# Kernel tuning notes

Hardware: AMD Instinct MI355X
Metric: run time of the kernel (lower is better)

The kernel has to match this reference:

```python
import jax, jax.numpy as jnp
import numpy as np

N, D, H, B, E = 100000, 256, 256, 128, 128
STEPS = 5


def setup_inputs() -> dict:
    key = jax.random.key(0)
    ks = jax.random.split(key, 16)
    w = lambda i, shape: (jax.random.normal(ks[i], shape, jnp.float32) * 0.05)
    inp = {
        "x": jax.random.normal(ks[0], (N, D), jnp.float32),
        "batch_idxs": jnp.sort(jax.random.randint(ks[1], (N,), 0, B)),
        # FNN: Linear(D,H) -> ELU -> Linear(H,H)
        "fnn_W1": w(2, (D, H)), "fnn_b1": jnp.zeros((H,), jnp.float32),
        "fnn_W2": w(3, (H, H)), "fnn_b2": jnp.zeros((H,), jnp.float32),
        # 3-layer LSTM, input 2H (layer 0) / H (layers 1,2), hidden H
        "Wih0": w(4, (4 * H, 2 * H)), "Whh0": w(5, (4 * H, H)),
        "bih0": jnp.zeros((4 * H,), jnp.float32), "bhh0": jnp.zeros((4 * H,), jnp.float32),
        "Wih1": w(6, (4 * H, H)), "Whh1": w(7, (4 * H, H)),
        "bih1": jnp.zeros((4 * H,), jnp.float32), "bhh1": jnp.zeros((4 * H,), jnp.float32),
        "Wih2": w(8, (4 * H, H)), "Whh2": w(9, (4 * H, H)),
        "bih2": jnp.zeros((4 * H,), jnp.float32), "bhh2": jnp.zeros((4 * H,), jnp.float32),
        # output Linear(2H, E)
        "out_W": w(10, (2 * H, E)), "out_b": jnp.zeros((E,), jnp.float32),
    }
    return inp


def _lstm_cell(xin, h, c, Wih, Whh, bih, bhh):
    gates = xin @ Wih.T + bih + h @ Whh.T + bhh  # (B, 4H)
    i, f, g, o = jnp.split(gates, 4, axis=-1)    # PyTorch gate order i,f,g,o
    c = jax.nn.sigmoid(f) * c + jax.nn.sigmoid(i) * jnp.tanh(g)
    h = jax.nn.sigmoid(o) * jnp.tanh(c)
    return h, c


def reference(x, batch_idxs, fnn_W1, fnn_b1, fnn_W2, fnn_b2,
              Wih0, Whh0, bih0, bhh0, Wih1, Whh1, bih1, bhh1,
              Wih2, Whh2, bih2, bhh2, out_W, out_b):
    # FNN (ELU between layers)
    hfeat = jax.nn.elu(x @ fnn_W1 + fnn_b1) @ fnn_W2 + fnn_b2  # (N, H)

    Wihs, Whhs = (Wih0, Wih1, Wih2), (Whh0, Whh1, Whh2)
    bihs, bhhs = (bih0, bih1, bih2), (bhh0, bhh1, bhh2)
    hs = [jnp.zeros((B, H), hfeat.dtype) for _ in range(3)]
    cs = [jnp.zeros((B, H), hfeat.dtype) for _ in range(3)]
    q_star = jnp.zeros((B, 2 * H), hfeat.dtype)

    for _ in range(STEPS):
        layer_in = q_star
        for l in range(3):
            hs[l], cs[l] = _lstm_cell(layer_in, hs[l], cs[l], Wihs[l], Whhs[l], bihs[l], bhhs[l])
            layer_in = hs[l]
        q = layer_in  # (B, H)
        # segment (per-graph) attention softmax over nodes
        e = jnp.sum(hfeat * q[batch_idxs], axis=-1)                     # (N,)
        m = jax.ops.segment_max(e, batch_idxs, num_segments=B)
        m = jnp.where(jnp.isfinite(m), m, 0.0)                          # guard empty segments
        ex = jnp.exp(e - m[batch_idxs])
        denom = jax.ops.segment_sum(ex, batch_idxs, num_segments=B) + 1e-16
        a = ex / denom[batch_idxs]                                      # (N,)
        r = jax.ops.segment_sum(a[:, None] * hfeat, batch_idxs, num_segments=B)  # (B, H)
        q_star = jnp.concatenate([q, r], axis=-1)                       # (B, 2H)

    return q_star @ out_W + out_b  # (B, E)
```

## Files before the change

kernel.cpp:

```cpp
#include <hip/hip_runtime.h>

#define NN 100000
#define NSTEP 5
#define LSTR 264

typedef unsigned short ushort_t;
typedef __attribute__((ext_vector_type(8))) short short8;
typedef __attribute__((ext_vector_type(4))) float floatx4;

__device__ __forceinline__ ushort_t f2bf(float f){
  union { float f; unsigned u; } v; v.f = f;
  unsigned r = v.u + 0x7fffu + ((v.u >> 16) & 1u);
  return (ushort_t)(r >> 16);
}
__device__ __forceinline__ float bf2f(ushort_t s){
  union { unsigned u; float f; } v; v.u = ((unsigned)s) << 16;
  return v.f;
}
__device__ __forceinline__ float sigf(float x){ return 1.0f/(1.0f+__expf(-x)); }

__global__ __launch_bounds__(512) void fnn_fused(const float* __restrict__ x,
    const ushort_t* __restrict__ W1P, const float* __restrict__ b1,
    const ushort_t* __restrict__ W2P, const float* __restrict__ b2,
    ushort_t* __restrict__ hfeat, int M)
{
  __shared__ ushort_t buf[64 * LSTR];
  int tid = threadIdx.x;
  int w = tid >> 6, lane = tid & 63, qd = lane >> 4, r16 = lane & 15;
  int row0 = blockIdx.x * 64;
  int col0 = w * 32;

  floatx4 acc[4][2];
  short8 afA[4], afB[4], bfA[2], bfB[2];

  auto LDA = [&](short8* d, int kc){
    #pragma unroll
    for (int i=0;i<4;i++) d[i] = *(const short8*)&buf[(i*16 + r16)*LSTR + kc*32 + qd*8];
  };
  auto LDW = [&](short8* d, const ushort_t* P, int kc){
    #pragma unroll
    for (int j=0;j<2;j++) d[j] = *(const short8*)(P + (size_t)(((w*2 + j)*8 + kc)*64 + lane)*8);
  };
  auto MM = [&](short8* a, short8* b){
    #pragma unroll
    for (int i=0;i<4;i++)
      #pragma unroll
      for (int j=0;j<2;j++)
        acc[i][j] = __builtin_amdgcn_mfma_f32_16x16x32_bf16(a[i], b[j], acc[i][j], 0, 0, 0);
  };

  {
    float4 xv[8];
    #pragma unroll
    for (int it = 0; it < 8; it++){
      int idx = it * 512 + tid;
      int rg = row0 + (idx >> 6); if (rg >= M) rg = M - 1;
      xv[it] = *(const float4*)(x + (size_t)rg * 256 + (idx & 63) * 4);
    }
    #pragma unroll
    for (int it = 0; it < 8; it++){
      int idx = it * 512 + tid;
      ushort4 pk = make_ushort4(f2bf(xv[it].x), f2bf(xv[it].y), f2bf(xv[it].z), f2bf(xv[it].w));
      *(ushort4*)&buf[(idx >> 6) * LSTR + (idx & 63) * 4] = pk;
    }
  }
  LDW(bfA, W1P, 0);
  __syncthreads();

  #pragma unroll
  for (int i=0;i<4;i++)
    #pragma unroll
    for (int j=0;j<2;j++) acc[i][j] = (floatx4){0.f,0.f,0.f,0.f};
  LDA(afA, 0);
  #pragma unroll
  for (int kc = 0; kc < 8; kc += 2){
    if (kc + 1 < 8){ LDA(afB, kc+1); LDW(bfB, W1P, kc+1); }
    MM(afA, bfA);
    if (kc + 2 < 8){ LDA(afA, kc+2); LDW(bfA, W1P, kc+2); }
    if (kc + 1 < 8) MM(afB, bfB);
  }
  __syncthreads();

  LDW(bfA, W2P, 0);
  #pragma unroll
  for (int i=0;i<4;i++){
    #pragma unroll
    for (int j=0;j<2;j++){
      int col = col0 + j*16 + r16;
      float bb = b1[col];
      #pragma unroll
      for (int rr=0;rr<4;rr++){
        int row = i*16 + qd*4 + rr;
        float v = acc[i][j][rr] + bb;
        v = v > 0.f ? v : (__expf(v) - 1.0f);
        buf[row * LSTR + col] = f2bf(v);
      }
    }
  }
  __syncthreads();

  #pragma unroll
  for (int i=0;i<4;i++)
    #pragma unroll
    for (int j=0;j<2;j++) acc[i][j] = (floatx4){0.f,0.f,0.f,0.f};
  LDA(afA, 0);
  #pragma unroll
  for (int kc = 0; kc < 8; kc += 2){
    if (kc + 1 < 8){ LDA(afB, kc+1); LDW(bfB, W2P, kc+1); }
    MM(afA, bfA);
    if (kc + 2 < 8){ LDA(afA, kc+2); LDW(bfA, W2P, kc+2); }
    if (kc + 1 < 8) MM(afB, bfB);
  }

  #pragma unroll
  for (int i=0;i<4;i++){
    #pragma unroll
    for (int j=0;j<2;j++){
      int col = col0 + j*16 + r16;
      float bb = b2[col];
      #pragma unroll
      for (int rr=0;rr<4;rr++){
        int row = row0 + i*16 + qd*4 + rr;
        if (row < M) hfeat[(size_t)row * 256 + col] = f2bf(acc[i][j][rr] + bb);
      }
    }
  }
}

template<int KC, bool FIN>
__global__ __launch_bounds__(256, 1) void lstm_layer(const ushort_t* __restrict__ A,
    const ushort_t* __restrict__ WcP, const float* __restrict__ bcp,
    float* __restrict__ c, ushort_t* __restrict__ dstA, int sA,
    ushort_t* __restrict__ dstB, int sB, float* __restrict__ qdst,
    const float* __restrict__ r_part, const float* __restrict__ z_part)
{
  __shared__ float sbuf[3][4][256];
  __shared__ ushort_t shr[16][264];
  constexpr int lda = KC * 32;
  constexpr int kcq = KC >> 2;
  int tid = threadIdx.x, w = tid >> 6, lane = tid & 63, qd = lane >> 4, r16 = lane & 15;
  int m0 = (blockIdx.x & 7) * 16, nt = blockIdx.x >> 3;

  if (FIN){
    int col = tid;
    #pragma unroll 4
    for (int r = 0; r < 16; r++){
      int bb = m0 + r;
      const float* rp = r_part + ((size_t)bb*256 + col)*8;
      float4 aa = *(const float4*)rp;
      float4 ab = *(const float4*)(rp + 4);
      float s = aa.x+aa.y+aa.z+aa.w + ab.x+ab.y+ab.z+ab.w;
      const float* zp = z_part + bb*8;
      float4 za = *(const float4*)zp;
      float4 zb = *(const float4*)(zp + 4);
      float z = za.x+za.y+za.z+za.w + zb.x+zb.y+zb.z+zb.w;
      shr[r][col] = f2bf(s / (z + 1e-16f));
    }
    __syncthreads();
  }

  int kc0 = w * kcq;
  floatx4 acc[4];
  #pragma unroll
  for (int g=0; g<4; g++) acc[g] = (floatx4){0.f,0.f,0.f,0.f};

  const ushort_t* Ar = A + (size_t)(m0 + r16) * lda + qd * 8;
  #pragma unroll
  for (int kk = 0; kk < kcq; kk++){
    int kc = kc0 + kk;
    short8 av;
    if (FIN && kc >= 8 && kc < 16)
      av = *(const short8*)&shr[r16][(kc - 8)*32 + qd*8];
    else
      av = *(const short8*)(Ar + kc*32);
    #pragma unroll
    for (int g = 0; g < 4; g++){
      short8 bv = *(const short8*)(WcP + (size_t)((((g*16 + nt)*KC) + kc)*64 + lane)*8);
      acc[g] = __builtin_amdgcn_mfma_f32_16x16x32_bf16(av, bv, acc[g], 0, 0, 0);
    }
  }
  if (w){
    #pragma unroll
    for (int g=0; g<4; g++) *(floatx4*)&sbuf[w-1][g][lane*4] = acc[g];
  }
  __syncthreads();
  if (w == 0){
    #pragma unroll
    for (int g=0; g<4; g++)
      #pragma unroll
      for (int t=0; t<3; t++){
        floatx4 p = *(floatx4*)&sbuf[t][g][lane*4];
        acc[g] = acc[g] + p;
      }
    int h = nt*16 + r16;
    float bci = bcp[h], bcf = bcp[256+h], bcg = bcp[512+h], bco = bcp[768+h];
    #pragma unroll
    for (int rr=0; rr<4; rr++){
      int row = m0 + qd*4 + rr;
      float gi = acc[0][rr] + bci;
      float gf = acc[1][rr] + bcf;
      float gg = acc[2][rr] + bcg;
      float go = acc[3][rr] + bco;
      float cp = c[row*256 + h];
      float cn = sigf(gf)*cp + sigf(gi)*tanhf(gg);
      float hn = sigf(go)*tanhf(cn);
      c[row*256 + h] = cn;
      ushort_t hb = f2bf(hn);
      dstA[row*sA + h] = hb;
      dstB[row*sB + h] = hb;
      if (qdst) qdst[row*512 + h] = hn;
    }
  }
}

__global__ __launch_bounds__(256) void attn_onepass(const ushort_t* __restrict__ hfeat,
    const int* __restrict__ seg, const float* __restrict__ q_star,
    float* __restrict__ r_part, float* __restrict__ z_part)
{
  __shared__ float sred[4][260];
  int b = blockIdx.x >> 3, p = blockIdx.x & 7;
  int w = threadIdx.x >> 6, lane = threadIdx.x & 63;
  int s0 = seg[b], s1 = seg[b+1], len = s1 - s0;
  int q0 = s0 + ((len * p) >> 3);
  int q1 = s0 + ((len * (p+1)) >> 3);

  float S0=0.f, S1=0.f, S2=0.f, S3=0.f, Z=0.f;
  float4 q = *(const float4*)(q_star + (size_t)b*512 + lane*4);

  ushort4 cur[4];
  int base = q0 + w;
  #pragma unroll
  for (int u=0;u<4;u++){
    int n = base + 4*u;
    cur[u] = (n < q1) ? *(const ushort4*)(hfeat + (size_t)n*256 + lane*4)
                      : make_ushort4(0,0,0,0);
  }
  for (; base < q1; base += 16){
    ushort4 nxt[4];
    #pragma unroll
    for (int u=0;u<4;u++){
      int n = base + 16 + 4*u;
      nxt[u] = (n < q1) ? *(const ushort4*)(hfeat + (size_t)n*256 + lane*4) : cur[u];
    }
    float fv[4][4], d[4];
    #pragma unroll
    for (int u=0;u<4;u++){
      fv[u][0]=bf2f(cur[u].x); fv[u][1]=bf2f(cur[u].y);
      fv[u][2]=bf2f(cur[u].z); fv[u][3]=bf2f(cur[u].w);
      d[u] = fv[u][0]*q.x + fv[u][1]*q.y + fv[u][2]*q.z + fv[u][3]*q.w;
    }
    #pragma unroll
    for (int off = 32; off; off >>= 1){
      #pragma unroll
      for (int u=0;u<4;u++) d[u] += __shfl_xor(d[u], off);
    }
    #pragma unroll
    for (int u=0;u<4;u++){
      if (base + 4*u < q1){
        float wt = __expf(d[u]);
        Z += wt;
        S0 += wt*fv[u][0]; S1 += wt*fv[u][1];
        S2 += wt*fv[u][2]; S3 += wt*fv[u][3];
      }
    }
    #pragma unroll
    for (int u=0;u<4;u++) cur[u] = nxt[u];
  }

  *(float4*)&sred[w][lane*4] = (float4){S0, S1, S2, S3};
  if (lane == 0) sred[w][256] = Z;
  __syncthreads();
  int f = threadIdx.x;
  if (f < 256){
    float v = sred[0][f] + sred[1][f] + sred[2][f] + sred[3][f];
    r_part[((size_t)b*256 + f)*8 + p] = v;
    if (f == 0)
      z_part[b*8 + p] = sred[0][256] + sred[1][256] + sred[2][256] + sred[3][256];
  }
}

__global__ __launch_bounds__(256) void attn_fin(const float* __restrict__ r_part,
    const float* __restrict__ z_part, const float* __restrict__ q_star,
    const float* __restrict__ outW, const float* __restrict__ outb,
    float* __restrict__ out)
{
  __shared__ float qs[512];
  int b = blockIdx.x, f = threadIdx.x;
  const float* rp = r_part + ((size_t)b*256 + f)*8;
  float4 aa = *(const float4*)rp;
  float4 ab = *(const float4*)(rp + 4);
  float s = aa.x+aa.y+aa.z+aa.w + ab.x+ab.y+ab.z+ab.w;
  const float* zp = z_part + b*8;
  float4 za = *(const float4*)zp;
  float4 zb = *(const float4*)(zp + 4);
  float z = za.x+za.y+za.z+za.w + zb.x+zb.y+zb.z+zb.w;
  qs[256 + f] = s / (z + 1e-16f);
  qs[f] = q_star[b*512 + f];
  __syncthreads();
  if (f < 128){
    float acc = outb[f];
    for (int k = 0; k < 512; k++) acc += qs[k] * outW[k*128 + f];
    out[b*128 + f] = acc;
  }
}

__global__ void prep_all(const float* __restrict__ W1, const float* __restrict__ W2,
    const float* __restrict__ Wih0, const float* __restrict__ Whh0,
    const float* __restrict__ Wih1, const float* __restrict__ Whh1,
    const float* __restrict__ Wih2, const float* __restrict__ Whh2,
    const float* __restrict__ bih0, const float* __restrict__ bhh0,
    const float* __restrict__ bih1, const float* __restrict__ bhh1,
    const float* __restrict__ bih2, const float* __restrict__ bhh2,
    const int* __restrict__ bidx,
    ushort_t* __restrict__ W1P, ushort_t* __restrict__ W2P,
    ushort_t* __restrict__ Wc0P, ushort_t* __restrict__ Wc1P, ushort_t* __restrict__ Wc2P,
    float* __restrict__ c, ushort_t* __restrict__ xc, float* __restrict__ q_star,
    float* __restrict__ bc, int* __restrict__ seg)
{
  int i = blockIdx.x*256 + threadIdx.x;
  if (i < 131072){
    const float* W = (i < 65536) ? W1 : W2;
    ushort_t* P = (i < 65536) ? W1P : W2P;
    int r = i & 65535;
    int T = r >> 12, r2 = r & 4095;
    int kc = r2 >> 9, l = (r2 >> 3) & 63, j = r2 & 7;
    int k = kc*32 + ((l>>4)<<3) + j;
    int n = T*16 + (l & 15);
    P[r] = f2bf(W[k*256 + n]);
    return;
  }
  i -= 131072;
  if (i < 786432){
    int T = i / 12288, r2 = i - T*12288;
    int kc = r2 >> 9, l = (r2 >> 3) & 63, j = r2 & 7;
    int k = kc*32 + ((l>>4)<<3) + j;
    int g = T >> 4, n = (T & 15)*16 + (l & 15);
    int row = g*256 + n;
    Wc0P[i] = f2bf(k < 512 ? Wih0[row*512 + k] : Whh0[row*256 + (k - 512)]);
    return;
  }
  i -= 786432;
  if (i < 1048576){
    const float* Wih = (i < 524288) ? Wih1 : Wih2;
    const float* Whh = (i < 524288) ? Whh1 : Whh2;
    ushort_t* P = (i < 524288) ? Wc1P : Wc2P;
    int r = i & 524287;
    int T = r >> 13, r2 = r & 8191;
    int kc = r2 >> 9, l = (r2 >> 3) & 63, j = r2 & 7;
    int k = kc*32 + ((l>>4)<<3) + j;
    int g = T >> 4, n = (T & 15)*16 + (l & 15);
    int row = g*256 + n;
    P[r] = f2bf(k < 256 ? Wih[row*256 + k] : Whh[row*256 + (k - 256)]);
    return;
  }
  i -= 1048576;
  if (i < 98304) { c[i] = 0.f; return; }
  i -= 98304;
  if (i < 229376) { xc[i] = 0; return; }
  i -= 229376;
  if (i < 65536) { q_star[i] = 0.f; return; }
  i -= 65536;
  if (i < 3072) {
    int l = i >> 10, g = i & 1023;
    const float* bi = (l == 0) ? bih0 : ((l == 1) ? bih1 : bih2);
    const float* bh = (l == 0) ? bhh0 : ((l == 1) ? bhh1 : bhh2);
    bc[i] = bi[g] + bh[g];
    return;
  }
  i -= 3072;
  if (i < 129) {
    int lo = 0, hi = NN;
    while (lo < hi){ int mid = (lo + hi) >> 1; if (bidx[mid] < i) lo = mid + 1; else hi = mid; }
    seg[i] = lo;
    return;
  }
}

extern "C" void kernel_launch(void* const* d_in, const int* in_sizes, int n_in,
                              void* d_out, int out_size, void* d_ws, size_t ws_size,
                              hipStream_t stream)
{
  const float* x    = (const float*)d_in[0];
  const int*   bidx = (const int*)  d_in[1];
  const float* W1   = (const float*)d_in[2];
  const float* b1   = (const float*)d_in[3];
  const float* W2   = (const float*)d_in[4];
  const float* b2   = (const float*)d_in[5];
  const float* Wih0 = (const float*)d_in[6];
  const float* Whh0 = (const float*)d_in[7];
  const float* bih0 = (const float*)d_in[8];
  const float* bhh0 = (const float*)d_in[9];
  const float* Wih1 = (const float*)d_in[10];
  const float* Whh1 = (const float*)d_in[11];
  const float* bih1 = (const float*)d_in[12];
  const float* bhh1 = (const float*)d_in[13];
  const float* Wih2 = (const float*)d_in[14];
  const float* Whh2 = (const float*)d_in[15];
  const float* bih2 = (const float*)d_in[16];
  const float* bhh2 = (const float*)d_in[17];
  const float* outW = (const float*)d_in[18];
  const float* outb = (const float*)d_in[19];

  char* p = (char*)d_ws;
  auto alloc = [&](size_t bytes)->char*{ char* r = p; p += (bytes + 255) & ~(size_t)255; return r; };
  ushort_t* hfeat  = (ushort_t*)alloc((size_t)NN*256*2);
  ushort_t* W1P    = (ushort_t*)alloc(65536*2);
  ushort_t* W2P    = (ushort_t*)alloc(65536*2);
  ushort_t* Wc0P   = (ushort_t*)alloc(786432*2);
  ushort_t* Wc1P   = (ushort_t*)alloc(524288*2);
  ushort_t* Wc2P   = (ushort_t*)alloc(524288*2);
  float*    bc     = (float*)   alloc(3072*4);
  float*    c_all  = (float*)   alloc(98304*4);
  ushort_t* xc     = (ushort_t*)alloc(229376*2);
  float*    q_star = (float*)   alloc(65536*4);
  float*    r_part = (float*)   alloc((size_t)128*256*8*4);
  float*    z_part = (float*)   alloc(128*8*4);
  int*      seg    = (int*)     alloc(129*4);

  ushort_t* xc0 = xc;
  ushort_t* xc1 = xc + 98304;
  ushort_t* xc2 = xc + 163840;
  float* c0 = c_all, *c1 = c_all + 32768, *c2 = c_all + 65536;
  float* bc0 = bc, *bc1 = bc + 1024, *bc2 = bc + 2048;

  prep_all<<<9229, 256, 0, stream>>>(W1, W2, Wih0, Whh0, Wih1, Whh1, Wih2, Whh2,
                                     bih0, bhh0, bih1, bhh1, bih2, bhh2, bidx,
                                     W1P, W2P, Wc0P, Wc1P, Wc2P,
                                     c_all, xc, q_star, bc, seg);

  fnn_fused<<<1563, 512, 0, stream>>>(x, W1P, b1, W2P, b2, hfeat, NN);

  for (int s = 0; s < NSTEP; s++){
    if (s == 0)
      lstm_layer<24,false><<<128, 256, 0, stream>>>(xc0, Wc0P, bc0, c0,
          xc0 + 512, 768, xc1, 512, nullptr, nullptr, nullptr);
    else
      lstm_layer<24,true><<<128, 256, 0, stream>>>(xc0, Wc0P, bc0, c0,
          xc0 + 512, 768, xc1, 512, nullptr, r_part, z_part);
    lstm_layer<16,false><<<128, 256, 0, stream>>>(xc1, Wc1P, bc1, c1,
        xc1 + 256, 512, xc2, 512, nullptr, nullptr, nullptr);
    lstm_layer<16,false><<<128, 256, 0, stream>>>(xc2, Wc2P, bc2, c2,
        xc2 + 256, 512, xc0, 768, q_star, nullptr, nullptr);
    attn_onepass<<<1024, 256, 0, stream>>>(hfeat, seg, q_star, r_part, z_part);
  }
  attn_fin<<<128, 256, 0, stream>>>(r_part, z_part, q_star, outW, outb, (float*)d_out);
}
```

Before: 448.1 us.

## Stage FNN weights into LDS via async global_load_lds with 32-row tiles

The fused FNN kernel now handles 32 rows per block instead of 64, doubling the grid to 3125 blocks. Weight fragments are streamed into a double-buffered LDS area with global_load_lds and manual vmcnt waits, instead of being loaded into registers. The second layer's weights are prefetched while the ELU epilogue runs. The tail bounds check is dropped because 100000 divides evenly by 32, and lstm_layer loses its min-blocks launch bound. The aim is more overlap of weight fetch with MFMA and higher occupancy, at the cost of less reuse of each weight fragment per block.

```diff
diff --git a/kernel.cpp b/kernel.cpp
--- a/kernel.cpp
+++ b/kernel.cpp
@@ -24,74 +24,94 @@
     const ushort_t* __restrict__ W2P, const float* __restrict__ b2,
     ushort_t* __restrict__ hfeat, int M)
 {
-  __shared__ ushort_t buf[64 * LSTR];
+  __shared__ ushort_t buf[32 * LSTR];
+  __shared__ ushort_t wst[2][8][2][512];
   int tid = threadIdx.x;
   int w = tid >> 6, lane = tid & 63, qd = lane >> 4, r16 = lane & 15;
-  int row0 = blockIdx.x * 64;
-  int col0 = w * 32;
-
-  floatx4 acc[4][2];
-  short8 afA[4], afB[4], bfA[2], bfB[2];
-
-  auto LDA = [&](short8* d, int kc){
-    #pragma unroll
-    for (int i=0;i<4;i++) d[i] = *(const short8*)&buf[(i*16 + r16)*LSTR + kc*32 + qd*8];
-  };
-  auto LDW = [&](short8* d, const ushort_t* P, int kc){
-    #pragma unroll
-    for (int j=0;j<2;j++) d[j] = *(const short8*)(P + (size_t)(((w*2 + j)*8 + kc)*64 + lane)*8);
-  };
-  auto MM = [&](short8* a, short8* b){
-    #pragma unroll
-    for (int i=0;i<4;i++)
-      #pragma unroll
-      for (int j=0;j<2;j++)
-        acc[i][j] = __builtin_amdgcn_mfma_f32_16x16x32_bf16(a[i], b[j], acc[i][j], 0, 0, 0);
-  };
+  size_t row0 = (size_t)blockIdx.x * 32;
+
+  typedef __attribute__((address_space(3))) unsigned int lds_u32;
+  typedef __attribute__((address_space(1))) const unsigned int glb_u32;
+
+  float bb1[2], bb2[2];
+  #pragma unroll
+  for (int j = 0; j < 2; j++){
+    int col = w*32 + j*16 + r16;
+    bb1[j] = b1[col];
+    bb2[j] = b2[col];
+  }
 
   {
-    float4 xv[8];
-    #pragma unroll
-    for (int it = 0; it < 8; it++){
+    float4 xv[4];
+    #pragma unroll
+    for (int it = 0; it < 4; it++){
       int idx = it * 512 + tid;
-      int rg = row0 + (idx >> 6); if (rg >= M) rg = M - 1;
-      xv[it] = *(const float4*)(x + (size_t)rg * 256 + (idx & 63) * 4);
-    }
-    #pragma unroll
-    for (int it = 0; it < 8; it++){
+      xv[it] = *(const float4*)(x + (row0 + (idx >> 6)) * 256 + (idx & 63) * 4);
+    }
+    #pragma unroll
+    for (int it = 0; it < 4; it++){
       int idx = it * 512 + tid;
       ushort4 pk = make_ushort4(f2bf(xv[it].x), f2bf(xv[it].y), f2bf(xv[it].z), f2bf(xv[it].w));
       *(ushort4*)&buf[(idx >> 6) * LSTR + (idx & 63) * 4] = pk;
     }
   }
-  LDW(bfA, W1P, 0);
-  __syncthreads();
-
-  #pragma unroll
-  for (int i=0;i<4;i++)
-    #pragma unroll
-    for (int j=0;j<2;j++) acc[i][j] = (floatx4){0.f,0.f,0.f,0.f};
-  LDA(afA, 0);
-  #pragma unroll
-  for (int kc = 0; kc < 8; kc += 2){
-    if (kc + 1 < 8){ LDA(afB, kc+1); LDW(bfB, W1P, kc+1); }
-    MM(afA, bfA);
-    if (kc + 2 < 8){ LDA(afA, kc+2); LDW(bfA, W1P, kc+2); }
-    if (kc + 1 < 8) MM(afB, bfB);
-  }
-  __syncthreads();
-
-  LDW(bfA, W2P, 0);
-  #pragma unroll
-  for (int i=0;i<4;i++){
+  __syncthreads();
+
+  auto STAGE = [&](const ushort_t* __restrict__ P, int kc, int ph){
+    #pragma unroll
+    for (int j = 0; j < 2; j++){
+      const ushort_t* gp = P + (size_t)(((w*2 + j)*8 + kc)*512) + lane*8;
+      __builtin_amdgcn_global_load_lds((glb_u32*)gp, (lds_u32*)&wst[ph][w][j][0], 16, 0, 0);
+    }
+  };
+
+  floatx4 acc[2][2];
+
+  auto GEMM = [&](const ushort_t* __restrict__ P, bool prestaged){
+    if (!prestaged){ STAGE(P, 0, 0); STAGE(P, 1, 1); }
+    #pragma unroll
+    for (int i=0;i<2;i++)
+      #pragma unroll
+      for (int j=0;j<2;j++) acc[i][j] = (floatx4){0.f,0.f,0.f,0.f};
+    #pragma unroll
+    for (int kc = 0; kc < 8; kc++){
+      int ph = kc & 1;
+      if (kc < 7) asm volatile("s_waitcnt vmcnt(2)" ::: "memory");
+      else        asm volatile("s_waitcnt vmcnt(0)" ::: "memory");
+      short8 af[2], bf[2];
+      #pragma unroll
+      for (int i=0;i<2;i++)
+        af[i] = *(const short8*)&buf[(i*16 + r16)*LSTR + kc*32 + qd*8];
+      #pragma unroll
+      for (int j=0;j<2;j++)
+        bf[j] = *(const short8*)&wst[ph][w][j][lane*8];
+      #pragma unroll
+      for (int i=0;i<2;i++)
+        #pragma unroll
+        for (int j=0;j<2;j++)
+          acc[i][j] = __builtin_amdgcn_mfma_f32_16x16x32_bf16(af[i], bf[j], acc[i][j], 0, 0, 0);
+      if (kc + 2 < 8){
+        asm volatile("s_waitcnt lgkmcnt(0)" ::: "memory");
+        STAGE(P, kc + 2, ph);
+      }
+    }
+  };
+
+  GEMM(W1P, false);
+
+  asm volatile("s_waitcnt lgkmcnt(0)" ::: "memory");
+  STAGE(W2P, 0, 0); STAGE(W2P, 1, 1);
+  __syncthreads();
+
+  #pragma unroll
+  for (int i=0;i<2;i++){
     #pragma unroll
     for (int j=0;j<2;j++){
-      int col = col0 + j*16 + r16;
-      float bb = b1[col];
+      int col = w*32 + j*16 + r16;
       #pragma unroll
       for (int rr=0;rr<4;rr++){
         int row = i*16 + qd*4 + rr;
-        float v = acc[i][j][rr] + bb;
+        float v = acc[i][j][rr] + bb1[j];
         v = v > 0.f ? v : (__expf(v) - 1.0f);
         buf[row * LSTR + col] = f2bf(v);
       }
@@ -99,36 +119,24 @@
   }
   __syncthreads();
 
-  #pragma unroll
-  for (int i=0;i<4;i++)
-    #pragma unroll
-    for (int j=0;j<2;j++) acc[i][j] = (floatx4){0.f,0.f,0.f,0.f};
-  LDA(afA, 0);
-  #pragma unroll
-  for (int kc = 0; kc < 8; kc += 2){
-    if (kc + 1 < 8){ LDA(afB, kc+1); LDW(bfB, W2P, kc+1); }
-    MM(afA, bfA);
-    if (kc + 2 < 8){ LDA(afA, kc+2); LDW(bfA, W2P, kc+2); }
-    if (kc + 1 < 8) MM(afB, bfB);
-  }
-
-  #pragma unroll
-  for (int i=0;i<4;i++){
+  GEMM(W2P, true);
+
+  #pragma unroll
+  for (int i=0;i<2;i++){
     #pragma unroll
     for (int j=0;j<2;j++){
-      int col = col0 + j*16 + r16;
-      float bb = b2[col];
+      int col = w*32 + j*16 + r16;
       #pragma unroll
       for (int rr=0;rr<4;rr++){
-        int row = row0 + i*16 + qd*4 + rr;
-        if (row < M) hfeat[(size_t)row * 256 + col] = f2bf(acc[i][j][rr] + bb);
+        size_t row = row0 + i*16 + qd*4 + rr;
+        hfeat[row * 256 + col] = f2bf(acc[i][j][rr] + bb2[j]);
       }
     }
   }
 }
 
 template<int KC, bool FIN>
-__global__ __launch_bounds__(256, 1) void lstm_layer(const ushort_t* __restrict__ A,
+__global__ __launch_bounds__(256) void lstm_layer(const ushort_t* __restrict__ A,
     const ushort_t* __restrict__ WcP, const float* __restrict__ bcp,
     float* __restrict__ c, ushort_t* __restrict__ dstA, int sA,
     ushort_t* __restrict__ dstB, int sB, float* __restrict__ qdst,
@@ -428,7 +436,7 @@
                                      W1P, W2P, Wc0P, Wc1P, Wc2P,
                                      c_all, xc, q_star, bc, seg);
 
-  fnn_fused<<<1563, 512, 0, stream>>>(x, W1P, b1, W2P, b2, hfeat, NN);
+  fnn_fused<<<3125, 512, 0, stream>>>(x, W1P, b1, W2P, b2, hfeat, NN);
 
   for (int s = 0; s < NSTEP; s++){
     if (s == 0)
```

Result: no change. 442.1 us (-1.3%).
